# Kernel optimization log

Hardware: AMD Instinct MI355X
Metric: run time of the kernel (lower is better)

The kernel has to match this reference:

```python
import jax, jax.numpy as jnp
import numpy as np

ALPHA = 1.0


def setup_inputs() -> dict:
    key = jax.random.key(0)
    ks = jax.random.split(key, 7)
    B, S, IN, OUT = 8, 8192, 1024, 1024
    RANK, DDIM, UDIM = 4, 100, 50
    return {
        "hidden_states": jax.random.normal(ks[0], (B, S, IN), dtype=jnp.float32),
        "W": jax.random.normal(ks[1], (OUT, IN), dtype=jnp.float32) * 0.02,
        "b": jax.random.normal(ks[2], (OUT,), dtype=jnp.float32) * 0.02,
        "lora_down": jax.random.normal(ks[3], (RANK, DDIM), dtype=jnp.float32) * 0.1,
        "lora_up": jax.random.normal(ks[4], (UDIM, RANK), dtype=jnp.float32) * 0.1,
        "down_aux": jax.random.normal(ks[5], (DDIM, IN), dtype=jnp.float32) * 0.03,
        "up_aux": jax.random.normal(ks[6], (OUT, UDIM), dtype=jnp.float32) * 0.03,
    }


def reference(hidden_states, W, b, lora_down, lora_up, down_aux, up_aux):
    # lilora_weight = up_aux @ lora_up @ lora_down @ down_aux  -> [out, in]
    lilora_weight = up_aux @ (lora_up @ (lora_down @ down_aux))
    base = jnp.einsum("bsi,oi->bso", hidden_states, W) + b
    delta = jnp.einsum("bsi,oi->bso", hidden_states, lilora_weight)
    return base + ALPHA * delta
```

## Files before the change

kernel.cpp:

```cpp
#include <hip/hip_runtime.h>
#include <hip/hip_bf16.h>
#include <stdint.h>

#define ALPHA 1.0f

typedef __attribute__((ext_vector_type(8))) short bf16x8;
typedef __attribute__((ext_vector_type(4))) float f32x4;
typedef unsigned short ushort_t;

__device__ __forceinline__ unsigned short f32_to_bf16_rne(float f) {
    union { float f; unsigned int u; } v; v.f = f;
    unsigned int u = v.u;
    unsigned int r = u + 0x7FFFu + ((u >> 16) & 1u);
    return (unsigned short)(r >> 16);
}

__device__ __forceinline__ unsigned int cvt_pk_bf16(float lo, float hi) {
    unsigned int r;
    asm("v_cvt_pk_bf16_f32 %0, %1, %2" : "=v"(r) : "v"(lo), "v"(hi));
    return r;
}

__device__ __forceinline__ void async_copy16(const void* g, void* l) {
    __builtin_amdgcn_global_load_lds(
        (const __attribute__((address_space(1))) void*)g,
        (__attribute__((address_space(3))) void*)l, 16, 0, 0);
}

template <bool BF16OUT>
__global__ __launch_bounds__(256)
void weff_fused_kernel(const float* __restrict__ W,
                       const float* __restrict__ lora_down,
                       const float* __restrict__ lora_up,
                       const float* __restrict__ down_aux,
                       const float* __restrict__ up_aux,
                       void* __restrict__ weff) {
    int o = blockIdx.x;
    int i0 = threadIdx.x * 4;

    float fac[4] = {0.f, 0.f, 0.f, 0.f};
    for (int u = 0; u < 50; ++u) {
        float ua = up_aux[o * 50 + u] * ALPHA;
#pragma unroll
        for (int r = 0; r < 4; ++r) fac[r] += ua * lora_up[u * 4 + r];
    }

    float4 t1[4];
#pragma unroll
    for (int r = 0; r < 4; ++r) t1[r] = make_float4(0.f, 0.f, 0.f, 0.f);
    for (int d = 0; d < 100; ++d) {
        float4 da = *(const float4*)(down_aux + d * 1024 + i0);
#pragma unroll
        for (int r = 0; r < 4; ++r) {
            float ld = lora_down[r * 100 + d];
            t1[r].x += ld * da.x; t1[r].y += ld * da.y;
            t1[r].z += ld * da.z; t1[r].w += ld * da.w;
        }
    }

    float4 acc = *(const float4*)(W + (long)o * 1024 + i0);
#pragma unroll
    for (int r = 0; r < 4; ++r) {
        acc.x += fac[r] * t1[r].x; acc.y += fac[r] * t1[r].y;
        acc.z += fac[r] * t1[r].z; acc.w += fac[r] * t1[r].w;
    }

    if (BF16OUT) {
        ushort4 rr;
        rr.x = f32_to_bf16_rne(acc.x); rr.y = f32_to_bf16_rne(acc.y);
        rr.z = f32_to_bf16_rne(acc.z); rr.w = f32_to_bf16_rne(acc.w);
        *(ushort4*)((ushort_t*)weff + (long)o * 1024 + i0) = rr;
    } else {
        *(float4*)((float*)weff + (long)o * 1024 + i0) = acc;
    }
}

#define BMM 256
#define BNN 256
#define BKK 64

__global__ __launch_bounds__(512, 2)
void gemm_fused_kernel(const float* __restrict__ A,
                       const ushort_t* __restrict__ Bt,
                       const float* __restrict__ bias,
                       float* __restrict__ C, int M, int N, int K) {
    __shared__ __align__(16) ushort_t Ab[2][BMM * BKK];
    __shared__ __align__(16) ushort_t Bb[2][BNN * BKK];

    int nTilesN = N / BNN;
    int nwg = gridDim.x;
    int bid = blockIdx.x;
    int swz = bid;
    if ((nwg & 7) == 0) {
        int cpx = nwg >> 3;
        swz = (bid & 7) * cpx + (bid >> 3);
    }
    int tm = swz / nTilesN;
    int tn = swz % nTilesN;
    const long rowA0 = (long)tm * BMM;
    const long colB0 = (long)tn * BNN;

    int tid = threadIdx.x;
    int lane = tid & 63;
    int wave = tid >> 6;
    int wr = wave >> 2;
    int wc = wave & 3;

    int amrow[2], amcol[2], amlds[2];
#pragma unroll
    for (int q = 0; q < 2; ++q) {
        int p = q * 512 + tid;
        amrow[q] = p >> 3;
        amcol[q] = p & 7;
        amlds[q] = amcol[q] ^ (amrow[q] & 7);
    }

    int prow[2], pcg[2];
#pragma unroll
    for (int q = 0; q < 2; ++q) {
        int pc = q * 512 + tid;
        prow[q] = pc >> 3;
        pcg[q] = (pc & 7) ^ (prow[q] & 7);
    }

    int fr = lane & 15;
    int h4 = lane >> 4;
    int s7 = fr & 7;
    int aoff = (wr * 128 + fr) * 64;
    int boff = (wc * 64 + fr) * 64;
    int ck[2] = { (h4 ^ s7) * 8, ((4 + h4) ^ s7) * 8 };

    f32x4 acc[8][4];
#pragma unroll
    for (int m = 0; m < 8; ++m)
#pragma unroll
        for (int n = 0; n < 4; ++n) acc[m][n] = (f32x4)(0.0f);

    const int nIter = K / BKK;

    float4 vP0[2], vP1[2], vQ0[2], vQ1[2];

    auto loadAh0 = [&](int kt) {
        const float* src = A + rowA0 * (long)K + kt * BKK;
#pragma unroll
        for (int q = 0; q < 2; ++q) {
            const float* gp = src + (long)amrow[q] * K + amcol[q] * 8;
            vP0[q] = ((const float4*)gp)[0];
            vP1[q] = ((const float4*)gp)[1];
        }
    };
    auto loadAh1 = [&](int kt) {
        const float* src = A + (rowA0 + 128) * (long)K + kt * BKK;
#pragma unroll
        for (int q = 0; q < 2; ++q) {
            const float* gp = src + (long)amrow[q] * K + amcol[q] * 8;
            vQ0[q] = ((const float4*)gp)[0];
            vQ1[q] = ((const float4*)gp)[1];
        }
    };
    auto writeAh0 = [&](int bufsel) {
        ushort_t* dst = &Ab[bufsel][0];
#pragma unroll
        for (int q = 0; q < 2; ++q) {
            uint4 w;
            w.x = cvt_pk_bf16(vP0[q].x, vP0[q].y);
            w.y = cvt_pk_bf16(vP0[q].z, vP0[q].w);
            w.z = cvt_pk_bf16(vP1[q].x, vP1[q].y);
            w.w = cvt_pk_bf16(vP1[q].z, vP1[q].w);
            *(uint4*)(dst + amrow[q] * 64 + amlds[q] * 8) = w;
        }
    };
    auto writeAh1 = [&](int bufsel) {
        ushort_t* dst = &Ab[bufsel][8192];
#pragma unroll
        for (int q = 0; q < 2; ++q) {
            uint4 w;
            w.x = cvt_pk_bf16(vQ0[q].x, vQ0[q].y);
            w.y = cvt_pk_bf16(vQ0[q].z, vQ0[q].w);
            w.z = cvt_pk_bf16(vQ1[q].x, vQ1[q].y);
            w.w = cvt_pk_bf16(vQ1[q].z, vQ1[q].w);
            *(uint4*)(dst + amrow[q] * 64 + amlds[q] * 8) = w;
        }
    };
    auto stageB = [&](int kt, int h, int bufsel) {
        const ushort_t* src = Bt + (colB0 + h * 128) * (long)K + kt * BKK;
        ushort_t* dst = &Bb[bufsel][h * 8192 + wave * 512];
#pragma unroll
        for (int q = 0; q < 2; ++q)
            async_copy16(src + (long)prow[q] * K + pcg[q] * 8, dst + q * 4096);
    };

    loadAh0(0); loadAh1(0);
    stageB(0, 0, 0); stageB(0, 1, 0);
    writeAh0(0);
    writeAh1(0);
    loadAh0(1); loadAh1(1);
    stageB(1, 0, 1); stageB(1, 1, 1);
    asm volatile("s_waitcnt vmcnt(12) lgkmcnt(0)" ::: "memory");
    __builtin_amdgcn_s_barrier();

#pragma unroll 1
    for (int j = 0; j < nIter; ++j) {
        int c = j & 1, o = c ^ 1;
        const ushort_t* Ac = &Ab[c][0];
        const ushort_t* Bc = &Bb[c][0];
        bool stage1 = (j + 1 < nIter);
        bool stage2 = (j + 2 < nIter);

        bf16x8 aL[4][2], aH[4][2], bL[2][2], bH[2][2];
#pragma unroll
        for (int m = 0; m < 4; ++m)
#pragma unroll
            for (int kk = 0; kk < 2; ++kk)
                aL[m][kk] = *(const bf16x8*)&Ac[aoff + m * 1024 + ck[kk]];
#pragma unroll
        for (int n = 0; n < 2; ++n)
#pragma unroll
            for (int kk = 0; kk < 2; ++kk)
                bL[n][kk] = *(const bf16x8*)&Bc[boff + n * 1024 + ck[kk]];

        __builtin_amdgcn_s_setprio(1);
#pragma unroll
        for (int m = 0; m < 4; ++m)
#pragma unroll
            for (int n = 0; n < 2; ++n)
#pragma unroll
                for (int kk = 0; kk < 2; ++kk)
                    acc[m][n] = __builtin_amdgcn_mfma_f32_16x16x32_bf16(
                        aL[m][kk], bL[n][kk], acc[m][n], 0, 0, 0);
        __builtin_amdgcn_s_setprio(0);

        if (stage1) writeAh0(o);

#pragma unroll
        for (int n = 0; n < 2; ++n)
#pragma unroll
            for (int kk = 0; kk < 2; ++kk)
                bH[n][kk] = *(const bf16x8*)&Bc[boff + (n + 2) * 1024 + ck[kk]];

        __builtin_amdgcn_s_setprio(1);
#pragma unroll
        for (int m = 0; m < 4; ++m)
#pragma unroll
            for (int n = 0; n < 2; ++n)
#pragma unroll
                for (int kk = 0; kk < 2; ++kk)
                    acc[m][n + 2] = __builtin_amdgcn_mfma_f32_16x16x32_bf16(
                        aL[m][kk], bH[n][kk], acc[m][n + 2], 0, 0, 0);
        __builtin_amdgcn_s_setprio(0);

#pragma unroll
        for (int m = 0; m < 4; ++m)
#pragma unroll
            for (int kk = 0; kk < 2; ++kk)
                aH[m][kk] = *(const bf16x8*)&Ac[aoff + (m + 4) * 1024 + ck[kk]];

        __builtin_amdgcn_s_setprio(1);
#pragma unroll
        for (int m = 0; m < 4; ++m)
#pragma unroll
            for (int n = 0; n < 2; ++n)
#pragma unroll
                for (int kk = 0; kk < 2; ++kk)
                    acc[m + 4][n + 2] = __builtin_amdgcn_mfma_f32_16x16x32_bf16(
                        aH[m][kk], bH[n][kk], acc[m + 4][n + 2], 0, 0, 0);
        __builtin_amdgcn_s_setprio(0);

        if (stage1) writeAh1(o);

        __builtin_amdgcn_s_barrier();

        if (stage2) {
            loadAh0(j + 2); loadAh1(j + 2);
            stageB(j + 2, 0, c); stageB(j + 2, 1, c);
        }

        __builtin_amdgcn_s_setprio(1);
#pragma unroll
        for (int m = 0; m < 4; ++m)
#pragma unroll
            for (int n = 0; n < 2; ++n)
#pragma unroll
                for (int kk = 0; kk < 2; ++kk)
                    acc[m + 4][n] = __builtin_amdgcn_mfma_f32_16x16x32_bf16(
                        aH[m][kk], bL[n][kk], acc[m + 4][n], 0, 0, 0);
        __builtin_amdgcn_s_setprio(0);

        if (stage2) {
            asm volatile("s_waitcnt vmcnt(12) lgkmcnt(0)" ::: "memory");
        } else {
            asm volatile("s_waitcnt vmcnt(0) lgkmcnt(0)" ::: "memory");
        }
        __builtin_amdgcn_s_barrier();
    }

    int ccol = lane & 15;
    int crow = (lane >> 4) * 4;
#pragma unroll
    for (int m = 0; m < 8; ++m) {
        long grow = rowA0 + wr * 128 + m * 16 + crow;
#pragma unroll
        for (int n = 0; n < 4; ++n) {
            long gcol = colB0 + wc * 64 + n * 16 + ccol;
            float bb = bias[gcol];
#pragma unroll
            for (int r = 0; r < 4; ++r) {
                C[(grow + r) * N + gcol] = acc[m][n][r] + bb;
            }
        }
    }
}

__global__ __launch_bounds__(256)
void gemm_f32_fallback(const float* __restrict__ A, const float* __restrict__ Bt,
                       const float* __restrict__ bias, float* __restrict__ C,
                       int M, int N, int K) {
    __shared__ float As[64][17];
    __shared__ float Bs[64][17];
    int tilesN = N / 64;
    int tm = blockIdx.x / tilesN;
    int tn = blockIdx.x % tilesN;
    int tid = threadIdx.x;
    int tr = tid / 16, tc = tid % 16;
    float acc[4][4] = {};
    for (int k0 = 0; k0 < K; k0 += 16) {
        for (int t = tid; t < 64 * 16; t += 256) {
            int r = t / 16, c = t % 16;
            As[r][c] = A[((long)tm * 64 + r) * K + k0 + c];
            Bs[r][c] = Bt[((long)tn * 64 + r) * K + k0 + c];
        }
        __syncthreads();
#pragma unroll
        for (int kk = 0; kk < 16; ++kk) {
            float av[4], bv[4];
#pragma unroll
            for (int i = 0; i < 4; ++i) av[i] = As[tr * 4 + i][kk];
#pragma unroll
            for (int j = 0; j < 4; ++j) bv[j] = Bs[tc * 4 + j][kk];
#pragma unroll
            for (int i = 0; i < 4; ++i)
#pragma unroll
                for (int j = 0; j < 4; ++j) acc[i][j] += av[i] * bv[j];
        }
        __syncthreads();
    }
#pragma unroll
    for (int i = 0; i < 4; ++i) {
        long row = (long)tm * 64 + tr * 4 + i;
#pragma unroll
        for (int j = 0; j < 4; ++j) {
            long col = (long)tn * 64 + tc * 4 + j;
            C[row * N + col] = acc[i][j] + bias[col];
        }
    }
}

extern "C" void kernel_launch(void* const* d_in, const int* in_sizes, int n_in,
                              void* d_out, int out_size, void* d_ws, size_t ws_size,
                              hipStream_t stream) {
    const float* hs        = (const float*)d_in[0];
    const float* W         = (const float*)d_in[1];
    const float* b         = (const float*)d_in[2];
    const float* lora_down = (const float*)d_in[3];
    const float* lora_up   = (const float*)d_in[4];
    const float* down_aux  = (const float*)d_in[5];
    const float* up_aux    = (const float*)d_in[6];
    float* out = (float*)d_out;

    const int K = 1024;
    const int N = 1024;
    const int M = in_sizes[0] / K;

    char* ws = (char*)d_ws;
    const size_t NEED_FAST = 2 * 1024 * 1024;

    if (ws_size >= NEED_FAST && (M % BMM) == 0) {
        ushort_t* weff = (ushort_t*)ws;
        weff_fused_kernel<true><<<N, 256, 0, stream>>>(W, lora_down, lora_up,
                                                       down_aux, up_aux, weff);
        int grid = (M / BMM) * (N / BNN);
        gemm_fused_kernel<<<grid, 512, 0, stream>>>(hs, weff, b, out, M, N, K);
    } else {
        float* weff = (float*)ws;
        weff_fused_kernel<false><<<N, 256, 0, stream>>>(W, lora_down, lora_up,
                                                        down_aux, up_aux, weff);
        int grid = (M / 64) * (N / 64);
        gemm_f32_fallback<<<grid, 256, 0, stream>>>(hs, weff, b, out, M, N, K);
    }
}
```

Baseline: 247.8 us.

## Load B fragments directly from global into registers, dropping LDS staging

```diff
diff --git a/kernel.cpp b/kernel.cpp
--- a/kernel.cpp
+++ b/kernel.cpp
@@ -19,12 +19,6 @@
     unsigned int r;
     asm("v_cvt_pk_bf16_f32 %0, %1, %2" : "=v"(r) : "v"(lo), "v"(hi));
     return r;
-}
-
-__device__ __forceinline__ void async_copy16(const void* g, void* l) {
-    __builtin_amdgcn_global_load_lds(
-        (const __attribute__((address_space(1))) void*)g,
-        (__attribute__((address_space(3))) void*)l, 16, 0, 0);
 }
 
 template <bool BF16OUT>
@@ -85,7 +79,6 @@
                        const float* __restrict__ bias,
                        float* __restrict__ C, int M, int N, int K) {
     __shared__ __align__(16) ushort_t Ab[2][BMM * BKK];
-    __shared__ __align__(16) ushort_t Bb[2][BNN * BKK];
 
     int nTilesN = N / BNN;
     int nwg = gridDim.x;
@@ -115,21 +108,14 @@
         amlds[q] = amcol[q] ^ (amrow[q] & 7);
     }
 
-    int prow[2], pcg[2];
-#pragma unroll
-    for (int q = 0; q < 2; ++q) {
-        int pc = q * 512 + tid;
-        prow[q] = pc >> 3;
-        pcg[q] = (pc & 7) ^ (prow[q] & 7);
-    }
-
     int fr = lane & 15;
     int h4 = lane >> 4;
     int s7 = fr & 7;
     int aoff = (wr * 128 + fr) * 64;
-    int boff = (wc * 64 + fr) * 64;
     int ck[2] = { (h4 ^ s7) * 8, ((4 + h4) ^ s7) * 8 };
 
+    const ushort_t* bBase = Bt + (colB0 + wc * 64 + fr) * (long)K + h4 * 8;
+
     f32x4 acc[8][4];
 #pragma unroll
     for (int m = 0; m < 8; ++m)
@@ -139,6 +125,7 @@
     const int nIter = K / BKK;
 
     float4 vP0[2], vP1[2], vQ0[2], vQ1[2];
+    bf16x8 bL[2][2], bH[2][2];
 
     auto loadAh0 = [&](int kt) {
         const float* src = A + rowA0 * (long)K + kt * BKK;
@@ -182,42 +169,43 @@
             *(uint4*)(dst + amrow[q] * 64 + amlds[q] * 8) = w;
         }
     };
-    auto stageB = [&](int kt, int h, int bufsel) {
-        const ushort_t* src = Bt + (colB0 + h * 128) * (long)K + kt * BKK;
-        ushort_t* dst = &Bb[bufsel][h * 8192 + wave * 512];
-#pragma unroll
-        for (int q = 0; q < 2; ++q)
-            async_copy16(src + (long)prow[q] * K + pcg[q] * 8, dst + q * 4096);
+    auto loadBH = [&](int kt) {
+#pragma unroll
+        for (int n = 0; n < 2; ++n)
+#pragma unroll
+            for (int kk = 0; kk < 2; ++kk)
+                bH[n][kk] = *(const bf16x8*)(bBase + (long)(n + 2) * 16 * K +
+                                             kt * BKK + kk * 32);
+    };
+    auto loadBL = [&](int kt) {
+#pragma unroll
+        for (int n = 0; n < 2; ++n)
+#pragma unroll
+            for (int kk = 0; kk < 2; ++kk)
+                bL[n][kk] = *(const bf16x8*)(bBase + (long)n * 16 * K +
+                                             kt * BKK + kk * 32);
     };
 
     loadAh0(0); loadAh1(0);
-    stageB(0, 0, 0); stageB(0, 1, 0);
-    writeAh0(0);
-    writeAh1(0);
+    writeAh0(0); writeAh1(0);
+    loadBH(0); loadBL(0);
     loadAh0(1); loadAh1(1);
-    stageB(1, 0, 1); stageB(1, 1, 1);
-    asm volatile("s_waitcnt vmcnt(12) lgkmcnt(0)" ::: "memory");
+    asm volatile("s_waitcnt lgkmcnt(0)" ::: "memory");
     __builtin_amdgcn_s_barrier();
 
 #pragma unroll 1
     for (int j = 0; j < nIter; ++j) {
         int c = j & 1, o = c ^ 1;
         const ushort_t* Ac = &Ab[c][0];
-        const ushort_t* Bc = &Bb[c][0];
-        bool stage1 = (j + 1 < nIter);
-        bool stage2 = (j + 2 < nIter);
-
-        bf16x8 aL[4][2], aH[4][2], bL[2][2], bH[2][2];
+        bool w1 = (j + 1 < nIter);
+        bool l2 = (j + 2 < nIter);
+
+        bf16x8 a[4][2];
 #pragma unroll
         for (int m = 0; m < 4; ++m)
 #pragma unroll
             for (int kk = 0; kk < 2; ++kk)
-                aL[m][kk] = *(const bf16x8*)&Ac[aoff + m * 1024 + ck[kk]];
-#pragma unroll
-        for (int n = 0; n < 2; ++n)
-#pragma unroll
-            for (int kk = 0; kk < 2; ++kk)
-                bL[n][kk] = *(const bf16x8*)&Bc[boff + n * 1024 + ck[kk]];
+                a[m][kk] = *(const bf16x8*)&Ac[aoff + m * 1024 + ck[kk]];
 
         __builtin_amdgcn_s_setprio(1);
 #pragma unroll
@@ -227,16 +215,10 @@
 #pragma unroll
                 for (int kk = 0; kk < 2; ++kk)
                     acc[m][n] = __builtin_amdgcn_mfma_f32_16x16x32_bf16(
-                        aL[m][kk], bL[n][kk], acc[m][n], 0, 0, 0);
+                        a[m][kk], bL[n][kk], acc[m][n], 0, 0, 0);
         __builtin_amdgcn_s_setprio(0);
 
-        if (stage1) writeAh0(o);
-
-#pragma unroll
-        for (int n = 0; n < 2; ++n)
-#pragma unroll
-            for (int kk = 0; kk < 2; ++kk)
-                bH[n][kk] = *(const bf16x8*)&Bc[boff + (n + 2) * 1024 + ck[kk]];
+        if (w1) writeAh0(o);
 
         __builtin_amdgcn_s_setprio(1);
 #pragma unroll
@@ -246,14 +228,14 @@
 #pragma unroll
                 for (int kk = 0; kk < 2; ++kk)
                     acc[m][n + 2] = __builtin_amdgcn_mfma_f32_16x16x32_bf16(
-                        aL[m][kk], bH[n][kk], acc[m][n + 2], 0, 0, 0);
+                        a[m][kk], bH[n][kk], acc[m][n + 2], 0, 0, 0);
         __builtin_amdgcn_s_setprio(0);
 
 #pragma unroll
         for (int m = 0; m < 4; ++m)
 #pragma unroll
             for (int kk = 0; kk < 2; ++kk)
-                aH[m][kk] = *(const bf16x8*)&Ac[aoff + (m + 4) * 1024 + ck[kk]];
+                a[m][kk] = *(const bf16x8*)&Ac[aoff + (m + 4) * 1024 + ck[kk]];
 
         __builtin_amdgcn_s_setprio(1);
 #pragma unroll
@@ -263,16 +245,12 @@
 #pragma unroll
                 for (int kk = 0; kk < 2; ++kk)
                     acc[m + 4][n + 2] = __builtin_amdgcn_mfma_f32_16x16x32_bf16(
-                        aH[m][kk], bH[n][kk], acc[m + 4][n + 2], 0, 0, 0);
+                        a[m][kk], bH[n][kk], acc[m + 4][n + 2], 0, 0, 0);
         __builtin_amdgcn_s_setprio(0);
 
-        if (stage1) writeAh1(o);
-
-        __builtin_amdgcn_s_barrier();
-
-        if (stage2) {
-            loadAh0(j + 2); loadAh1(j + 2);
-            stageB(j + 2, 0, c); stageB(j + 2, 1, c);
+        if (w1) {
+            writeAh1(o);
+            loadBH(j + 1);
         }
 
         __builtin_amdgcn_s_setprio(1);
@@ -283,14 +261,13 @@
 #pragma unroll
                 for (int kk = 0; kk < 2; ++kk)
                     acc[m + 4][n] = __builtin_amdgcn_mfma_f32_16x16x32_bf16(
-                        aH[m][kk], bL[n][kk], acc[m + 4][n], 0, 0, 0);
+                        a[m][kk], bL[n][kk], acc[m + 4][n], 0, 0, 0);
         __builtin_amdgcn_s_setprio(0);
 
-        if (stage2) {
-            asm volatile("s_waitcnt vmcnt(12) lgkmcnt(0)" ::: "memory");
-        } else {
-            asm volatile("s_waitcnt vmcnt(0) lgkmcnt(0)" ::: "memory");
-        }
+        if (w1) loadBL(j + 1);
+        if (l2) { loadAh0(j + 2); loadAh1(j + 2); }
+
+        asm volatile("s_waitcnt lgkmcnt(0)" ::: "memory");
         __builtin_amdgcn_s_barrier();
     }
 
```

Result: no change. 248.2 us (+0.2%).
